# Kernel tuning notes

Measured on AMD Instinct MI355X. Metric: run time of the kernel, lower is better.

The kernel has to match this reference:

```python
import jax, jax.numpy as jnp
import numpy as np
from math import factorial, sqrt

L = 8
RCUT = 5.0
PI = 3.14159  # literal used in the torch module's Ylm normalization
N_POINTS = 4194304


def powcmplx(zr, zi, n):
    # Faithful port, including the n>2 recurrence that uses the *updated*
    # real part when forming the imaginary part (as in the source).
    if n == 0:
        return jnp.ones_like(zr), jnp.zeros_like(zr)
    if n == 1:
        return zr, zi
    if n == 2:
        return zr * zr - zi * zi, 2.0 * zr * zi
    r, im = zr, zi
    for _ in range(2, n + 1):
        r = zr * r - zi * im
        im = zr * im + zi * r  # uses updated r, matching the source exactly
    return r, im


def _forward(pos):
    norms = jnp.sqrt(jnp.sum(pos * pos, axis=1))
    valid = norms > 0
    mask = valid.astype(pos.dtype)
    safe = jnp.where(valid, norms, 1.0)
    # cosine_cutoff uses the true pi (acos trick in the source)
    cut = 0.5 * (jnp.cos(norms * (jnp.pi / RCUT)) + 1.0)
    cut = jnp.where(norms > RCUT, 0.0, cut) * mask  # mask replaces boolean row-select
    xp_r = -0.5 * pos[:, 0]
    xp_i = -0.5 * pos[:, 1]
    xm_r = 0.5 * pos[:, 0]
    xm_i = -0.5 * pos[:, 1]
    x0 = pos[:, 2]
    n_out = (L + 1) ** 2
    vals = [jnp.zeros((), pos.dtype)] * n_out
    i = 0
    for l in range(L + 1):
        w_l = cut / safe ** l * sqrt((2 * l + 1) / 4 / PI)  # per-point weight for this l
        for M in range(-l, 1):
            m = abs(M)
            sr = jnp.zeros_like(x0)
            si = jnp.zeros_like(x0)
            for p in range(l + 1):
                q = p - m
                s = l - p - q
                if q >= 0 and s >= 0:
                    z1r, z1i = powcmplx(xp_r, xp_i, p)
                    z2r, z2i = powcmplx(xm_r, xm_i, q)
                    zr = z1r ** 2 - z2i ** 2      # faithful to source (squared terms)
                    zi = z1r * z2i + z1i * z2r
                    c = 1.0 / (factorial(p) * factorial(q) * factorial(s))
                    sr = sr + zr * x0 * c          # source multiplies by x0 (x0**s is unused there)
                    si = si + zi * x0 * c
            f = sqrt(factorial(l + m) * factorial(l - m))
            w = f * w_l
            clm_r = jnp.sum(sr * w)
            clm_i = jnp.sum(si * w)
            if m == 0:
                vals[i] = clm_r
            else:
                fac = sqrt(2.0) * (-1) ** m
                vals[i] = fac * clm_i
                vals[i + 2 * m] = fac * clm_r
            i += 1
        i += l
    return jnp.stack(vals).reshape(-1, 1)


def setup_inputs() -> dict:
    key = jax.random.key(0)
    pos = jax.random.normal(key, (N_POINTS, 3), dtype=jnp.float32) * 2.0
    return {"pos": pos}


def reference(pos):
    return _forward(pos)
```

## Files before the change

kernel.cpp:

```cpp
#include <hip/hip_runtime.h>
#include <math.h>


typedef float f32x2 __attribute__((ext_vector_type(2)));

#define NL 8
#define NBLK 1024
#define NTHR 256

__device__ __forceinline__ f32x2 sp(float v) { return f32x2{v, v}; }

__device__ __forceinline__ f32x2 pkfma(f32x2 a, f32x2 b, f32x2 c) {
    return __builtin_elementwise_fma(a, b, c);
}

__device__ __forceinline__ float waveReduce(float v) {
    v += __shfl_down(v, 32);
    v += __shfl_down(v, 16);
    v += __shfl_down(v, 8);
    v += __shfl_down(v, 4);
    v += __shfl_down(v, 2);
    v += __shfl_down(v, 1);
    return v;
}

__device__ __forceinline__ void point_body_lo(float x, float y, float z,
                                              float* __restrict__ acc0,
                                              f32x2* __restrict__ accp) {
    const float FACT[9] = {1.f, 1.f, 2.f, 6.f, 24.f, 120.f, 720.f, 5040.f, 40320.f};

    const float r2 = x * x + y * y + z * z;
    const bool valid = r2 > 0.0f;
    const float inv0 = __builtin_amdgcn_rsqf(r2);
    const float norm = r2 * inv0;
    float cut = 0.5f * (__cosf(norm * 0.6283185307179586f) + 1.0f);
    cut = (r2 > 25.0f) ? 0.0f : cut;
    cut = valid ? cut : 0.0f;
    const float inv = valid ? inv0 : 1.0f;
    const float x0c = z * cut;

    const f32x2 w  = { -0.5f * x,  0.5f * x };
    const f32x2 wi = { -0.5f * y, -0.5f * y };

    f32x2 zr[6], zi[6];
    zr[0] = sp(1.f); zi[0] = sp(0.f);
    zr[1] = w;       zi[1] = wi;
    zr[2] = w * w - wi * wi;
    zi[2] = (w + w) * wi;
    {
        f32x2 cr = zr[2];
        f32x2 ci = w * wi + wi * cr;
#pragma unroll
        for (int k = 3; k <= 5; ++k) {
            const f32x2 nr = w * cr - wi * ci;
            const f32x2 ni = w * ci + wi * nr;
            cr = nr; ci = ni;
            zr[k] = nr; zi[k] = ni;
        }
    }

    float aa[6], bb[6], cc[6], dd[6], sqa[6];
#pragma unroll
    for (int p = 0; p <= 5; ++p) {
        aa[p] = zr[p].x;  cc[p] = zr[p].y;
        bb[p] = zi[p].x;  dd[p] = zi[p].y;
        sqa[p] = aa[p] * aa[p];
    }

    float h[9];
    h[0] = x0c;
#pragma unroll
    for (int l = 1; l <= NL; ++l) h[l] = h[l - 1] * inv;

    {
        float Y0[5];
#pragma unroll
        for (int p = 0; p <= 4; ++p) {
            const float cpq = 1.0f / (FACT[p] * FACT[p]);
            Y0[p] = fmaf(-dd[p], dd[p], sqa[p]) * cpq;
        }
#pragma unroll
        for (int l = 0; l <= NL; ++l) {
            float sr = 0.f;
#pragma unroll
            for (int p = 0; p <= 4; ++p) {
                if (2 * p <= l) {
                    const float is = 1.0f / FACT[l - 2 * p];
                    sr = fmaf(Y0[p], is, sr);
                }
            }
            acc0[l] = fmaf(sr, h[l], acc0[l]);
        }
    }

#pragma unroll
    for (int m = 1; m <= 2; ++m) {
        f32x2 Y[6];
#pragma unroll
        for (int p = 0; p <= 5; ++p) {
            if (p >= m && 2 * p - m <= NL) {
                const int q = p - m;
                const float cpq = 1.0f / (FACT[p] * FACT[q]);
                const float bc = bb[p] * cc[q];
                const f32x2 A = { -dd[q], aa[p] };
                const f32x2 B = {  dd[q], dd[q] };
                const f32x2 C = { sqa[p], bc };
                Y[p] = pkfma(A, B, C) * sp(cpq);
            }
        }
#pragma unroll
        for (int l = m; l <= NL; ++l) {
            f32x2 s = sp(0.f);
#pragma unroll
            for (int p = 0; p <= 5; ++p) {
                if (p >= m && 2 * p - m <= l) {
                    const float is = 1.0f / FACT[l - 2 * p + m];
                    s = pkfma(Y[p], sp(is), s);
                }
            }
            const int ai = (m == 1) ? (l - 1) : (l + 6);
            accp[ai] = pkfma(s, sp(h[l]), accp[ai]);
        }
    }
}

__device__ __forceinline__ void point_body_hi(float x, float y, float z,
                                              f32x2* __restrict__ accp) {
    const float FACT[9] = {1.f, 1.f, 2.f, 6.f, 24.f, 120.f, 720.f, 5040.f, 40320.f};

    const float r2 = x * x + y * y + z * z;
    const bool valid = r2 > 0.0f;
    const float inv0 = __builtin_amdgcn_rsqf(r2);
    const float norm = r2 * inv0;
    float cut = 0.5f * (__cosf(norm * 0.6283185307179586f) + 1.0f);
    cut = (r2 > 25.0f) ? 0.0f : cut;
    cut = valid ? cut : 0.0f;
    const float inv = valid ? inv0 : 1.0f;
    const float x0c = z * cut;

    const f32x2 w  = { -0.5f * x,  0.5f * x };
    const f32x2 wi = { -0.5f * y, -0.5f * y };

    f32x2 zr[9], zi[9];
    zr[0] = sp(1.f); zi[0] = sp(0.f);
    zr[1] = w;       zi[1] = wi;
    zr[2] = w * w - wi * wi;
    zi[2] = (w + w) * wi;
    {
        f32x2 cr = zr[2];
        f32x2 ci = w * wi + wi * cr;
#pragma unroll
        for (int k = 3; k <= NL; ++k) {
            const f32x2 nr = w * cr - wi * ci;
            const f32x2 ni = w * ci + wi * nr;
            cr = nr; ci = ni;
            zr[k] = nr; zi[k] = ni;
        }
    }

    float aa[9], bb[9], sqa[9], cc[3], dd[3];
#pragma unroll
    for (int p = 0; p <= NL; ++p) {
        if (p >= 3) {
            aa[p] = zr[p].x;  bb[p] = zi[p].x;
            sqa[p] = aa[p] * aa[p];
        }
        if (p <= 2) {
            cc[p] = zr[p].y;  dd[p] = zi[p].y;
        }
    }

    float h[9];
    h[0] = x0c;
#pragma unroll
    for (int l = 1; l <= NL; ++l) h[l] = h[l - 1] * inv;

#pragma unroll
    for (int m = 3; m <= NL; ++m) {
        const int baseB[9] = {0, 0, 0, 0, 6, 11, 15, 18, 20};
        f32x2 Y[9];
#pragma unroll
        for (int p = 0; p <= NL; ++p) {
            if (p >= m && 2 * p - m <= NL) {
                const int q = p - m;
                const float cpq = 1.0f / (FACT[p] * FACT[q]);
                const float bc = bb[p] * cc[q];
                const f32x2 A = { -dd[q], aa[p] };
                const f32x2 B = {  dd[q], dd[q] };
                const f32x2 C = { sqa[p], bc };
                Y[p] = pkfma(A, B, C) * sp(cpq);
            }
        }
#pragma unroll
        for (int l = m; l <= NL; ++l) {
            f32x2 s = sp(0.f);
#pragma unroll
            for (int p = 0; p <= NL; ++p) {
                if (p >= m && 2 * p - m <= l) {
                    const float is = 1.0f / FACT[l - 2 * p + m];
                    s = pkfma(Y[p], sp(is), s);
                }
            }
            const int ai = baseB[m] + (l - m);
            accp[ai] = pkfma(s, sp(h[l]), accp[ai]);
        }
    }
}

__global__ __launch_bounds__(256, 4)
void sht_lo(const float* __restrict__ pos, float* __restrict__ ws, int n) {
    float acc0[9];
    f32x2 accp[15];
#pragma unroll
    for (int i = 0; i < 9; ++i) acc0[i] = 0.f;
#pragma unroll
    for (int i = 0; i < 15; ++i) accp[i] = sp(0.f);

    const int t = blockIdx.x * NTHR + threadIdx.x;
    const int nthreads = NBLK * NTHR;
    const int nchunks = (n / 8 + nthreads - 1) / nthreads;

    for (int c = 0; c < nchunks; ++c) {
        const int idx = (c * nthreads + t) * 8;
#pragma unroll 1
        for (int k = 0; k < 8; ++k) {
            const int i = idx + k;
            float x, y, z;
            if (i < n) {
                x = pos[3 * i + 0];
                y = pos[3 * i + 1];
                z = pos[3 * i + 2];
            } else {
                x = 0.f; y = 0.f; z = 0.f;
            }
            point_body_lo(x, y, z, acc0, accp);
        }
    }

    __shared__ float red[81][5];
    const int lane = threadIdx.x & 63;
    const int wave = threadIdx.x >> 6;

#pragma unroll
    for (int l = 0; l <= NL; ++l) {
        float vr = waveReduce(acc0[l]);
        if (lane == 0) red[l * l + l][wave] = vr;
    }
#pragma unroll
    for (int m = 1; m <= 2; ++m) {
#pragma unroll
        for (int l = m; l <= NL; ++l) {
            const int ai = (m == 1) ? (l - 1) : (l + 6);
            float vr = waveReduce(accp[ai].x);
            if (lane == 0) red[l * l + l + m][wave] = vr;
            float vi = waveReduce(accp[ai].y);
            if (lane == 0) red[l * l + l - m][wave] = vi;
        }
    }
    __syncthreads();

    if ((int)threadIdx.x < 81) {
        const int j = threadIdx.x;
        int l = 0;
        while ((l + 1) * (l + 1) <= j) ++l;
        const int M = j - l * l - l;
        const int am = (M < 0) ? -M : M;
        if (am <= 2) {
            float s = 0.f;
#pragma unroll
            for (int w2 = 0; w2 < 4; ++w2) s += red[j][w2];
            ws[(size_t)j * NBLK + blockIdx.x] = s;
        }
    }
}

__global__ __launch_bounds__(256, 4)
void sht_hi(const float* __restrict__ pos, float* __restrict__ ws, int n) {
    f32x2 accp[21];
#pragma unroll
    for (int i = 0; i < 21; ++i) accp[i] = sp(0.f);

    const int t = blockIdx.x * NTHR + threadIdx.x;
    const int nthreads = NBLK * NTHR;
    const int nchunks = (n / 8 + nthreads - 1) / nthreads;

    for (int c = 0; c < nchunks; ++c) {
        const int idx = (c * nthreads + t) * 8;
#pragma unroll 1
        for (int k = 0; k < 8; ++k) {
            const int i = idx + k;
            float x, y, z;
            if (i < n) {
                x = pos[3 * i + 0];
                y = pos[3 * i + 1];
                z = pos[3 * i + 2];
            } else {
                x = 0.f; y = 0.f; z = 0.f;
            }
            point_body_hi(x, y, z, accp);
        }
    }

    __shared__ float red[81][5];
    const int lane = threadIdx.x & 63;
    const int wave = threadIdx.x >> 6;

#pragma unroll
    for (int m = 3; m <= NL; ++m) {
        const int baseB[9] = {0, 0, 0, 0, 6, 11, 15, 18, 20};
#pragma unroll
        for (int l = m; l <= NL; ++l) {
            const int ai = baseB[m] + (l - m);
            float vr = waveReduce(accp[ai].x);
            if (lane == 0) red[l * l + l + m][wave] = vr;
            float vi = waveReduce(accp[ai].y);
            if (lane == 0) red[l * l + l - m][wave] = vi;
        }
    }
    __syncthreads();

    if ((int)threadIdx.x < 81) {
        const int j = threadIdx.x;
        int l = 0;
        while ((l + 1) * (l + 1) <= j) ++l;
        const int M = j - l * l - l;
        const int am = (M < 0) ? -M : M;
        if (am >= 3) {
            float s = 0.f;
#pragma unroll
            for (int w2 = 0; w2 < 4; ++w2) s += red[j][w2];
            ws[(size_t)j * NBLK + blockIdx.x] = s;
        }
    }
}

__device__ double dfact(int nn) {
    double r = 1.0;
    for (int i = 2; i <= nn; ++i) r *= (double)i;
    return r;
}

__global__ __launch_bounds__(256)
void sht_finalize(const float* __restrict__ ws, float* __restrict__ out) {
    const int j = blockIdx.x;
    const int t = threadIdx.x;
    float s = 0.f;
#pragma unroll
    for (int k = 0; k < NBLK / 256; ++k)
        s += ws[(size_t)j * NBLK + k * 256 + t];
    s = waveReduce(s);

    __shared__ float red[4];
    const int lane = t & 63, wave = t >> 6;
    if (lane == 0) red[wave] = s;
    __syncthreads();
    if (t == 0) {
        float tot = red[0] + red[1] + red[2] + red[3];
        int l = 0;
        while ((l + 1) * (l + 1) <= j) ++l;
        const int M = j - l * l - l;
        const int m = (M < 0) ? -M : M;
        double sc = sqrt(dfact(l + m) * dfact(l - m)) *
                    sqrt((double)(2 * l + 1) / (4.0 * 3.14159));
        if (m > 0) sc *= sqrt(2.0) * ((m & 1) ? -1.0 : 1.0);
        out[j] = (float)((double)tot * sc);
    }
}

extern "C" void kernel_launch(void* const* d_in, const int* in_sizes, int n_in,
                              void* d_out, int out_size, void* d_ws, size_t ws_size,
                              hipStream_t stream) {
    const float* pos = (const float*)d_in[0];
    const int npts = in_sizes[0] / 3;
    float* ws = (float*)d_ws;
    float* out = (float*)d_out;

    sht_lo<<<NBLK, NTHR, 0, stream>>>(pos, ws, npts);
    sht_hi<<<NBLK, NTHR, 0, stream>>>(pos, ws, npts);
    sht_finalize<<<81, 256, 0, stream>>>(ws, out);
}
```

Measured before the change: 147.8 us.

## Pack two points per thread into packed-FP32 lanes instead of re/im packing

Result: faster. 143.2 us (-3.1%).

```diff
diff --git a/kernel.cpp b/kernel.cpp
--- a/kernel.cpp
+++ b/kernel.cpp
@@ -24,197 +24,193 @@
     return v;
 }
 
-__device__ __forceinline__ void point_body_lo(float x, float y, float z,
-                                              float* __restrict__ acc0,
-                                              f32x2* __restrict__ accp) {
-    const float FACT[9] = {1.f, 1.f, 2.f, 6.f, 24.f, 120.f, 720.f, 5040.f, 40320.f};
-
+__device__ __forceinline__ void prologue(float x, float y, float z,
+                                         float& inv, float& x0c) {
     const float r2 = x * x + y * y + z * z;
     const bool valid = r2 > 0.0f;
-    const float inv0 = __builtin_amdgcn_rsqf(r2);
-    const float norm = r2 * inv0;
+    const float iv0 = __builtin_amdgcn_rsqf(r2);
+    const float norm = r2 * iv0;
     float cut = 0.5f * (__cosf(norm * 0.6283185307179586f) + 1.0f);
     cut = (r2 > 25.0f) ? 0.0f : cut;
     cut = valid ? cut : 0.0f;
-    const float inv = valid ? inv0 : 1.0f;
-    const float x0c = z * cut;
-
-    const f32x2 w  = { -0.5f * x,  0.5f * x };
-    const f32x2 wi = { -0.5f * y, -0.5f * y };
-
-    f32x2 zr[6], zi[6];
+    inv = valid ? iv0 : 1.0f;
+    x0c = z * cut;
+}
+
+template <int KMAX>
+__device__ __forceinline__ void chainN(const f32x2 w, const f32x2 wi,
+                                       f32x2* __restrict__ zr,
+                                       f32x2* __restrict__ zi) {
     zr[0] = sp(1.f); zi[0] = sp(0.f);
-    zr[1] = w;       zi[1] = wi;
-    zr[2] = w * w - wi * wi;
-    zi[2] = (w + w) * wi;
-    {
+    if (KMAX >= 1) { zr[1] = w; zi[1] = wi; }
+    if (KMAX >= 2) {
+        zr[2] = w * w - wi * wi;
+        zi[2] = (w + w) * wi;
+    }
+    if (KMAX >= 3) {
         f32x2 cr = zr[2];
         f32x2 ci = w * wi + wi * cr;
 #pragma unroll
-        for (int k = 3; k <= 5; ++k) {
+        for (int k = 3; k <= KMAX; ++k) {
             const f32x2 nr = w * cr - wi * ci;
             const f32x2 ni = w * ci + wi * nr;
             cr = nr; ci = ni;
             zr[k] = nr; zi[k] = ni;
         }
     }
-
-    float aa[6], bb[6], cc[6], dd[6], sqa[6];
-#pragma unroll
-    for (int p = 0; p <= 5; ++p) {
-        aa[p] = zr[p].x;  cc[p] = zr[p].y;
-        bb[p] = zi[p].x;  dd[p] = zi[p].y;
-        sqa[p] = aa[p] * aa[p];
-    }
-
-    float h[9];
-    h[0] = x0c;
+}
+
+__device__ __forceinline__ void pair_body_lo(
+        float xA, float yA, float zA, float xB, float yB, float zB,
+        float* __restrict__ acc0,
+        float* __restrict__ accRe, float* __restrict__ accIm) {
+    const float FACT[9] = {1.f, 1.f, 2.f, 6.f, 24.f, 120.f, 720.f, 5040.f, 40320.f};
+
+    float invA, x0cA, invB, x0cB;
+    prologue(xA, yA, zA, invA, x0cA);
+    prologue(xB, yB, zB, invB, x0cB);
+    const f32x2 inv = {invA, invB};
+
+    const f32x2 wi = { -0.5f * yA, -0.5f * yB };
+    f32x2 z1r[6], z1i[6], z2r[4], z2i[4];
+    chainN<5>(f32x2{ -0.5f * xA, -0.5f * xB }, wi, z1r, z1i);
+    chainN<3>(f32x2{  0.5f * xA,  0.5f * xB }, wi, z2r, z2i);
+
+    f32x2 sqa[6];
+#pragma unroll
+    for (int p = 0; p <= 5; ++p) sqa[p] = z1r[p] * z1r[p];
+
+    f32x2 h[9];
+    h[0] = f32x2{x0cA, x0cB};
 #pragma unroll
     for (int l = 1; l <= NL; ++l) h[l] = h[l - 1] * inv;
 
+    f32x2 z2r4, z2i4;
     {
-        float Y0[5];
+        const f32x2 w2 = {  0.5f * xA,  0.5f * xB };
+        const f32x2 nr = w2 * z2r[3] - wi * z2i[3];
+        const f32x2 ni = w2 * z2i[3] + wi * nr;
+        z2r4 = nr; z2i4 = ni;
+    }
+    {
+        f32x2 Y0[5];
 #pragma unroll
         for (int p = 0; p <= 4; ++p) {
             const float cpq = 1.0f / (FACT[p] * FACT[p]);
-            Y0[p] = fmaf(-dd[p], dd[p], sqa[p]) * cpq;
+            const f32x2 dd = (p <= 3) ? z2i[p] : z2i4;
+            Y0[p] = pkfma(-dd, dd, sqa[p]) * sp(cpq);
         }
 #pragma unroll
         for (int l = 0; l <= NL; ++l) {
-            float sr = 0.f;
+            f32x2 sr = sp(0.f);
 #pragma unroll
             for (int p = 0; p <= 4; ++p) {
                 if (2 * p <= l) {
                     const float is = 1.0f / FACT[l - 2 * p];
-                    sr = fmaf(Y0[p], is, sr);
+                    sr = pkfma(Y0[p], sp(is), sr);
                 }
             }
-            acc0[l] = fmaf(sr, h[l], acc0[l]);
+            acc0[l] = fmaf(sr.x, h[l].x, acc0[l]);
+            acc0[l] = fmaf(sr.y, h[l].y, acc0[l]);
         }
     }
 
 #pragma unroll
     for (int m = 1; m <= 2; ++m) {
-        f32x2 Y[6];
+        f32x2 Yr[6], Yi[6];
 #pragma unroll
         for (int p = 0; p <= 5; ++p) {
             if (p >= m && 2 * p - m <= NL) {
                 const int q = p - m;
                 const float cpq = 1.0f / (FACT[p] * FACT[q]);
-                const float bc = bb[p] * cc[q];
-                const f32x2 A = { -dd[q], aa[p] };
-                const f32x2 B = {  dd[q], dd[q] };
-                const f32x2 C = { sqa[p], bc };
-                Y[p] = pkfma(A, B, C) * sp(cpq);
+                Yr[p] = pkfma(-z2i[q], z2i[q], sqa[p]) * sp(cpq);
+                Yi[p] = pkfma(z1r[p], z2i[q], z1i[p] * z2r[q]) * sp(cpq);
             }
         }
 #pragma unroll
         for (int l = m; l <= NL; ++l) {
-            f32x2 s = sp(0.f);
+            f32x2 sr = sp(0.f), si = sp(0.f);
 #pragma unroll
             for (int p = 0; p <= 5; ++p) {
                 if (p >= m && 2 * p - m <= l) {
                     const float is = 1.0f / FACT[l - 2 * p + m];
-                    s = pkfma(Y[p], sp(is), s);
+                    sr = pkfma(Yr[p], sp(is), sr);
+                    si = pkfma(Yi[p], sp(is), si);
                 }
             }
             const int ai = (m == 1) ? (l - 1) : (l + 6);
-            accp[ai] = pkfma(s, sp(h[l]), accp[ai]);
-        }
-    }
-}
-
-__device__ __forceinline__ void point_body_hi(float x, float y, float z,
-                                              f32x2* __restrict__ accp) {
+            accRe[ai] = fmaf(sr.x, h[l].x, accRe[ai]);
+            accRe[ai] = fmaf(sr.y, h[l].y, accRe[ai]);
+            accIm[ai] = fmaf(si.x, h[l].x, accIm[ai]);
+            accIm[ai] = fmaf(si.y, h[l].y, accIm[ai]);
+        }
+    }
+}
+
+__device__ __forceinline__ void pair_body_hi(
+        float xA, float yA, float zA, float xB, float yB, float zB,
+        float* __restrict__ accRe, float* __restrict__ accIm) {
     const float FACT[9] = {1.f, 1.f, 2.f, 6.f, 24.f, 120.f, 720.f, 5040.f, 40320.f};
 
-    const float r2 = x * x + y * y + z * z;
-    const bool valid = r2 > 0.0f;
-    const float inv0 = __builtin_amdgcn_rsqf(r2);
-    const float norm = r2 * inv0;
-    float cut = 0.5f * (__cosf(norm * 0.6283185307179586f) + 1.0f);
-    cut = (r2 > 25.0f) ? 0.0f : cut;
-    cut = valid ? cut : 0.0f;
-    const float inv = valid ? inv0 : 1.0f;
-    const float x0c = z * cut;
-
-    const f32x2 w  = { -0.5f * x,  0.5f * x };
-    const f32x2 wi = { -0.5f * y, -0.5f * y };
-
-    f32x2 zr[9], zi[9];
-    zr[0] = sp(1.f); zi[0] = sp(0.f);
-    zr[1] = w;       zi[1] = wi;
-    zr[2] = w * w - wi * wi;
-    zi[2] = (w + w) * wi;
-    {
-        f32x2 cr = zr[2];
-        f32x2 ci = w * wi + wi * cr;
-#pragma unroll
-        for (int k = 3; k <= NL; ++k) {
-            const f32x2 nr = w * cr - wi * ci;
-            const f32x2 ni = w * ci + wi * nr;
-            cr = nr; ci = ni;
-            zr[k] = nr; zi[k] = ni;
-        }
-    }
-
-    float aa[9], bb[9], sqa[9], cc[3], dd[3];
-#pragma unroll
-    for (int p = 0; p <= NL; ++p) {
-        if (p >= 3) {
-            aa[p] = zr[p].x;  bb[p] = zi[p].x;
-            sqa[p] = aa[p] * aa[p];
-        }
-        if (p <= 2) {
-            cc[p] = zr[p].y;  dd[p] = zi[p].y;
-        }
-    }
-
-    float h[9];
-    h[0] = x0c;
+    float invA, x0cA, invB, x0cB;
+    prologue(xA, yA, zA, invA, x0cA);
+    prologue(xB, yB, zB, invB, x0cB);
+    const f32x2 inv = {invA, invB};
+
+    const f32x2 wi = { -0.5f * yA, -0.5f * yB };
+    f32x2 z1r[9], z1i[9], z2r[3], z2i[3];
+    chainN<8>(f32x2{ -0.5f * xA, -0.5f * xB }, wi, z1r, z1i);
+    chainN<2>(f32x2{  0.5f * xA,  0.5f * xB }, wi, z2r, z2i);
+
+    f32x2 sqa[9];
+#pragma unroll
+    for (int p = 3; p <= NL; ++p) sqa[p] = z1r[p] * z1r[p];
+
+    f32x2 h[9];
+    h[0] = f32x2{x0cA, x0cB};
 #pragma unroll
     for (int l = 1; l <= NL; ++l) h[l] = h[l - 1] * inv;
 
 #pragma unroll
     for (int m = 3; m <= NL; ++m) {
         const int baseB[9] = {0, 0, 0, 0, 6, 11, 15, 18, 20};
-        f32x2 Y[9];
-#pragma unroll
-        for (int p = 0; p <= NL; ++p) {
+        f32x2 Yr[9], Yi[9];
+#pragma unroll
+        for (int p = 3; p <= NL; ++p) {
             if (p >= m && 2 * p - m <= NL) {
                 const int q = p - m;
                 const float cpq = 1.0f / (FACT[p] * FACT[q]);
-                const float bc = bb[p] * cc[q];
-                const f32x2 A = { -dd[q], aa[p] };
-                const f32x2 B = {  dd[q], dd[q] };
-                const f32x2 C = { sqa[p], bc };
-                Y[p] = pkfma(A, B, C) * sp(cpq);
+                Yr[p] = pkfma(-z2i[q], z2i[q], sqa[p]) * sp(cpq);
+                Yi[p] = pkfma(z1r[p], z2i[q], z1i[p] * z2r[q]) * sp(cpq);
             }
         }
 #pragma unroll
         for (int l = m; l <= NL; ++l) {
-            f32x2 s = sp(0.f);
-#pragma unroll
-            for (int p = 0; p <= NL; ++p) {
+            f32x2 sr = sp(0.f), si = sp(0.f);
+#pragma unroll
+            for (int p = 3; p <= NL; ++p) {
                 if (p >= m && 2 * p - m <= l) {
                     const float is = 1.0f / FACT[l - 2 * p + m];
-                    s = pkfma(Y[p], sp(is), s);
+                    sr = pkfma(Yr[p], sp(is), sr);
+                    si = pkfma(Yi[p], sp(is), si);
                 }
             }
             const int ai = baseB[m] + (l - m);
-            accp[ai] = pkfma(s, sp(h[l]), accp[ai]);
-        }
-    }
-}
-
-__global__ __launch_bounds__(256, 4)
+            accRe[ai] = fmaf(sr.x, h[l].x, accRe[ai]);
+            accRe[ai] = fmaf(sr.y, h[l].y, accRe[ai]);
+            accIm[ai] = fmaf(si.x, h[l].x, accIm[ai]);
+            accIm[ai] = fmaf(si.y, h[l].y, accIm[ai]);
+        }
+    }
+}
+
+__global__ __launch_bounds__(256, 2)
 void sht_lo(const float* __restrict__ pos, float* __restrict__ ws, int n) {
-    float acc0[9];
-    f32x2 accp[15];
+    float acc0[9], accRe[15], accIm[15];
 #pragma unroll
     for (int i = 0; i < 9; ++i) acc0[i] = 0.f;
 #pragma unroll
-    for (int i = 0; i < 15; ++i) accp[i] = sp(0.f);
+    for (int i = 0; i < 15; ++i) { accRe[i] = 0.f; accIm[i] = 0.f; }
 
     const int t = blockIdx.x * NTHR + threadIdx.x;
     const int nthreads = NBLK * NTHR;
@@ -223,17 +219,12 @@
     for (int c = 0; c < nchunks; ++c) {
         const int idx = (c * nthreads + t) * 8;
 #pragma unroll 1
-        for (int k = 0; k < 8; ++k) {
-            const int i = idx + k;
-            float x, y, z;
-            if (i < n) {
-                x = pos[3 * i + 0];
-                y = pos[3 * i + 1];
-                z = pos[3 * i + 2];
-            } else {
-                x = 0.f; y = 0.f; z = 0.f;
-            }
-            point_body_lo(x, y, z, acc0, accp);
+        for (int k = 0; k < 8; k += 2) {
+            const int iA = idx + k, iB = idx + k + 1;
+            float xA = 0.f, yA = 0.f, zA = 0.f, xB = 0.f, yB = 0.f, zB = 0.f;
+            if (iA < n) { xA = pos[3 * iA]; yA = pos[3 * iA + 1]; zA = pos[3 * iA + 2]; }
+            if (iB < n) { xB = pos[3 * iB]; yB = pos[3 * iB + 1]; zB = pos[3 * iB + 2]; }
+            pair_body_lo(xA, yA, zA, xB, yB, zB, acc0, accRe, accIm);
         }
     }
 
@@ -251,9 +242,9 @@
 #pragma unroll
         for (int l = m; l <= NL; ++l) {
             const int ai = (m == 1) ? (l - 1) : (l + 6);
-            float vr = waveReduce(accp[ai].x);
+            float vr = waveReduce(accRe[ai]);
             if (lane == 0) red[l * l + l + m][wave] = vr;
-            float vi = waveReduce(accp[ai].y);
+            float vi = waveReduce(accIm[ai]);
             if (lane == 0) red[l * l + l - m][wave] = vi;
         }
     }
@@ -274,11 +265,11 @@
     }
 }
 
-__global__ __launch_bounds__(256, 4)
+__global__ __launch_bounds__(256, 2)
 void sht_hi(const float* __restrict__ pos, float* __restrict__ ws, int n) {
-    f32x2 accp[21];
-#pragma unroll
-    for (int i = 0; i < 21; ++i) accp[i] = sp(0.f);
+    float accRe[21], accIm[21];
+#pragma unroll
+    for (int i = 0; i < 21; ++i) { accRe[i] = 0.f; accIm[i] = 0.f; }
 
     const int t = blockIdx.x * NTHR + threadIdx.x;
     const int nthreads = NBLK * NTHR;
@@ -287,17 +278,12 @@
     for (int c = 0; c < nchunks; ++c) {
         const int idx = (c * nthreads + t) * 8;
 #pragma unroll 1
-        for (int k = 0; k < 8; ++k) {
-            const int i = idx + k;
-            float x, y, z;
-            if (i < n) {
-                x = pos[3 * i + 0];
-                y = pos[3 * i + 1];
-                z = pos[3 * i + 2];
-            } else {
-                x = 0.f; y = 0.f; z = 0.f;
-            }
-            point_body_hi(x, y, z, accp);
+        for (int k = 0; k < 8; k += 2) {
+            const int iA = idx + k, iB = idx + k + 1;
+            float xA = 0.f, yA = 0.f, zA = 0.f, xB = 0.f, yB = 0.f, zB = 0.f;
+            if (iA < n) { xA = pos[3 * iA]; yA = pos[3 * iA + 1]; zA = pos[3 * iA + 2]; }
+            if (iB < n) { xB = pos[3 * iB]; yB = pos[3 * iB + 1]; zB = pos[3 * iB + 2]; }
+            pair_body_hi(xA, yA, zA, xB, yB, zB, accRe, accIm);
         }
     }
 
@@ -311,9 +297,9 @@
 #pragma unroll
         for (int l = m; l <= NL; ++l) {
             const int ai = baseB[m] + (l - m);
-            float vr = waveReduce(accp[ai].x);
+            float vr = waveReduce(accRe[ai]);
             if (lane == 0) red[l * l + l + m][wave] = vr;
-            float vi = waveReduce(accp[ai].y);
+            float vi = waveReduce(accIm[ai]);
             if (lane == 0) red[l * l + l - m][wave] = vi;
         }
     }
```
